# Optimization experiments

Hardware: AMD Instinct MI355X
Metric: run time of the kernel (lower is better)

The kernel has to match this reference:

```python
import jax, jax.numpy as jnp
import numpy as np

D_MODEL = 192
D_STATE = 16
D_CONV = 4
EXPAND = 2
HEADDIM = 16
D_INNER = EXPAND * D_MODEL          # 384
NHEADS = D_INNER // HEADDIM         # 24
NGROUPS = 1
CHUNK = 256
BATCH = 2
SEQLEN = 8192
D_IN_PROJ = 2 * D_INNER + NGROUPS * D_STATE + NHEADS   # 808
D_IN_PROJ_B = NGROUPS * D_STATE                         # 16
CONV_DIM = D_INNER + NGROUPS * D_STATE                  # 400
EPS = 1e-5


def silu(x):
    return x * jax.nn.sigmoid(x)


def causal_dwconv(x, w, b):
    # x: (B, L, C), w: (C, 1, K) depthwise, b: (C,). Causal: left-pad K-1.
    C = x.shape[-1]
    xt = jnp.transpose(x, (0, 2, 1))  # (B, C, L)
    y = jax.lax.conv_general_dilated(
        xt, w, window_strides=(1,), padding=[(D_CONV - 1, 0)],
        dimension_numbers=('NCH', 'OIH', 'NCH'), feature_group_count=C)
    return jnp.transpose(y + b[None, :, None], (0, 2, 1))


def segsum(x):
    # x: (..., T) -> (..., T, T) lower-triangular segment sums (exclusive of j, inclusive of i)
    T = x.shape[-1]
    cs = jnp.cumsum(x, axis=-1)
    seg = cs[..., :, None] - cs[..., None, :]
    mask = jnp.tril(jnp.ones((T, T), dtype=bool))
    return jnp.where(mask, seg, -jnp.inf)


def ssd(x, dt, A, Bm, Cm):
    # Mamba2 chunked selective scan (mamba_chunk_scan_combined semantics).
    # x:(b,l,h,p) dt:(b,l,h) A:(h,) Bm,Cm:(b,l,g,n)
    b, l, h, p = x.shape
    g = Bm.shape[2]
    Bm = jnp.repeat(Bm, h // g, axis=2)  # (b,l,h,n)
    Cm = jnp.repeat(Cm, h // g, axis=2)
    nchunks = l // CHUNK
    tochunk = lambda t: t.reshape(b, nchunks, CHUNK, *t.shape[2:])
    xc, dtc, Bc, Cc = map(tochunk, (x, dt, Bm, Cm))
    a = jnp.transpose(dtc * A, (0, 3, 1, 2))        # (b,h,c,cl)
    a_cum = jnp.cumsum(a, axis=-1)                   # (b,h,c,cl)
    Lmat = jnp.exp(segsum(a))                        # (b,h,c,cl,cl)
    xdt = xc * dtc[..., None]                        # (b,c,cl,h,p)
    # intra-chunk (diagonal) output
    Y_diag = jnp.einsum('bclhn,bcshn,bhcls,bcshp->bclhp', Cc, Bc, Lmat, xdt)
    # per-chunk end states
    decay_states = jnp.exp(a_cum[..., -1:] - a_cum)  # (b,h,c,cl)
    states = jnp.einsum('bclhn,bhcl,bclhp->bchpn', Bc, decay_states, xdt)
    # inter-chunk recurrence (associative, via chunk-level segsum)
    init = jnp.zeros_like(states[:, :1])
    states = jnp.concatenate([init, states], axis=1)              # (b,c+1,h,p,n)
    a_chunk = jnp.pad(a_cum[..., -1], ((0, 0), (0, 0), (1, 0)))   # (b,h,c+1)
    decay_chunk = jnp.exp(segsum(a_chunk))                        # (b,h,c+1,c+1)
    states = jnp.einsum('bhzc,bchpn->bzhpn', decay_chunk, states)[:, :-1]  # (b,c,h,p,n)
    # state -> output within each chunk
    Y_off = jnp.einsum('bclhn,bchpn,bhcl->bclhp', Cc, states, jnp.exp(a_cum))
    return (Y_diag + Y_off).reshape(b, l, h, p)


def setup_inputs() -> dict:
    key = jax.random.key(0)
    ks = jax.random.split(key, 12)
    rng = np.random.default_rng(0)
    u = jax.random.normal(ks[0], (BATCH, SEQLEN, D_MODEL), dtype=jnp.float32)
    support = jax.random.normal(ks[1], (BATCH, SEQLEN, D_MODEL), dtype=jnp.float32)
    W_in = jax.random.normal(ks[2], (D_IN_PROJ, D_MODEL), dtype=jnp.float32) * 0.02
    W_in_b = jax.random.normal(ks[3], (D_IN_PROJ_B, D_MODEL), dtype=jnp.float32) * 0.02
    conv_w = jax.random.normal(ks[4], (CONV_DIM, 1, D_CONV), dtype=jnp.float32) * 0.2
    conv_b = jnp.zeros((CONV_DIM,), dtype=jnp.float32)
    conv_w_b = jax.random.normal(ks[5], (D_IN_PROJ_B, 1, D_CONV), dtype=jnp.float32) * 0.2
    conv_b_b = jnp.zeros((D_IN_PROJ_B,), dtype=jnp.float32)
    # dt_bias init per the module (inverse-softplus of dt in [1e-3, 1e-1])
    dt = np.exp(rng.uniform(size=(NHEADS,)) * (np.log(0.1) - np.log(0.001)) + np.log(0.001))
    dt = np.clip(dt, 1e-4, None)
    dt_bias = jnp.asarray(dt + np.log(-np.expm1(-dt)), dtype=jnp.float32)
    A_log = jnp.asarray(np.log(rng.uniform(1.0, 16.0, size=(NHEADS,))), dtype=jnp.float32)
    D = jnp.ones((NHEADS,), dtype=jnp.float32)
    norm_w = jnp.ones((D_INNER,), dtype=jnp.float32)
    W_out = jax.random.normal(ks[6], (D_MODEL, D_INNER), dtype=jnp.float32) * 0.02
    return {'u': u, 'support': support, 'W_in': W_in, 'W_in_b': W_in_b,
            'conv_w': conv_w, 'conv_b': conv_b, 'conv_w_b': conv_w_b, 'conv_b_b': conv_b_b,
            'dt_bias': dt_bias, 'A_log': A_log, 'D': D, 'norm_w': norm_w, 'W_out': W_out}


def reference(u, support, W_in, W_in_b, conv_w, conv_b, conv_w_b, conv_b_b,
              dt_bias, A_log, D, norm_w, W_out):
    bsz, l, _ = u.shape
    zxbdt = u @ W_in.T                                  # (b,l,808)
    c = support @ W_in_b.T                              # (b,l,16)
    z = zxbdt[..., :D_INNER]
    xB = zxbdt[..., D_INNER:D_INNER + CONV_DIM]
    dt = jax.nn.softplus(zxbdt[..., -NHEADS:] + dt_bias)  # (b,l,h)
    A = -jnp.exp(A_log)
    xB = silu(causal_dwconv(xB, conv_w, conv_b))
    Cv = silu(causal_dwconv(c, conv_w_b, conv_b_b))
    x = xB[..., :D_INNER]
    Bv = xB[..., D_INNER:]
    xh = x.reshape(bsz, l, NHEADS, HEADDIM)
    Bg = Bv.reshape(bsz, l, NGROUPS, D_STATE)
    Cg = Cv.reshape(bsz, l, NGROUPS, D_STATE)
    y = ssd(xh, dt, A, Bg, Cg) + D[None, None, :, None] * xh
    y = y.reshape(bsz, l, D_INNER)
    # RMSNormGated, norm_before_gate=False: normalize(y * silu(z)) * weight
    yg = y * silu(z)
    yn = yg * jax.lax.rsqrt(jnp.mean(yg * yg, axis=-1, keepdims=True) + EPS) * norm_w
    return yn @ W_out.T
```

## Files before the change

kernel.cpp:

```cpp
#include <hip/hip_runtime.h>
#include <cmath>

#define ROWS      16384
#define SEQLEN    8192
#define BATCH     2
#define NHEADS    24
#define HEADDIM   16
#define D_STATE   16
#define D_INNER   384
#define D_MODEL   192
#define D_IN_PROJ 808
#define CONV_DIM  400
#define NCHUNKS   32
#define CHUNK     256
#define EPS       1e-5f
#define LOG2E     1.44269504088896f

typedef short bf16x8 __attribute__((ext_vector_type(8)));
typedef short bf16x4 __attribute__((ext_vector_type(4)));
typedef float f32x4  __attribute__((ext_vector_type(4)));
typedef unsigned short us4v __attribute__((ext_vector_type(4)));
typedef unsigned short us8v __attribute__((ext_vector_type(8)));
typedef unsigned int  u32x4 __attribute__((ext_vector_type(4)));

#if __has_builtin(__builtin_amdgcn_mfma_f32_16x16x16bf16_1k)
#define MFMA16(a, b, c) __builtin_amdgcn_mfma_f32_16x16x16bf16_1k((a), (b), (c), 0, 0, 0)
#define HAVE_MFMA16 1
#elif __has_builtin(__builtin_amdgcn_mfma_f32_16x16x16_bf16)
#define MFMA16(a, b, c) __builtin_amdgcn_mfma_f32_16x16x16_bf16((a), (b), (c), 0, 0, 0)
#define HAVE_MFMA16 1
#else
#define HAVE_MFMA16 0
#endif

__device__ __forceinline__ float silu_f(float x) { return x / (1.0f + expf(-x)); }
__device__ __forceinline__ float softplus_f(float x) { return (x > 20.0f) ? x : log1pf(expf(x)); }
__device__ __forceinline__ unsigned short f2bf(float x) {
  unsigned u = __builtin_bit_cast(unsigned, x);
  u += 0x7fff + ((u >> 16) & 1);
  return (unsigned short)(u >> 16);
}
__device__ __forceinline__ float bf2f(unsigned short s) {
  unsigned u = (unsigned)s << 16;
  return __builtin_bit_cast(float, u);
}
__device__ __forceinline__ unsigned pk_bf(float a, float b) {
  unsigned ua = __builtin_bit_cast(unsigned, a) + 0x7fffu;
  unsigned ub = __builtin_bit_cast(unsigned, b) + 0x7fffu;
  return __builtin_amdgcn_perm(ub, ua, 0x07060302u);
}

__global__ __launch_bounds__(256)
void cvt3_kernel(const float* __restrict__ a, unsigned short* __restrict__ ao, long na,
                 const float* __restrict__ b, unsigned short* __restrict__ bo, long nb,
                 const float* __restrict__ c, unsigned short* __restrict__ co, long nc) {
  const long t0 = na >> 2, t1 = t0 + (nb >> 2), t2 = t1 + (nc >> 2);
  const long stride = (long)gridDim.x * blockDim.x;
  for (long i = (long)blockIdx.x * blockDim.x + threadIdx.x; i < t2; i += stride) {
    const float4* s; us4v* d; long j;
    if (i < t0)      { s = (const float4*)a; d = (us4v*)ao; j = i; }
    else if (i < t1) { s = (const float4*)b; d = (us4v*)bo; j = i - t0; }
    else             { s = (const float4*)c; d = (us4v*)co; j = i - t1; }
    float4 v = s[j];
    us4v o = { f2bf(v.x), f2bf(v.y), f2bf(v.z), f2bf(v.w) };
    d[j] = o;
  }
}

template<bool OUT_BF16, bool ROUTE>
__device__ __forceinline__
void gemm_body(unsigned short* __restrict__ As, unsigned short* __restrict__ Ws,
               const float* __restrict__ A, const unsigned short* __restrict__ W,
               void* __restrict__ Cp, int M, int N, int K, int bx, int by,
               unsigned short* __restrict__ zbuf, unsigned short* __restrict__ xT,
               unsigned short* __restrict__ Braw, unsigned short* __restrict__ draw) {
  constexpr int BM = 128, BN = 128, BK = 32, LDK = 40;
  const int tid  = threadIdx.x;
  const int wid  = tid >> 6, lane = tid & 63;
  const int wr   = wid >> 1, wc = wid & 1;
  const int fr   = lane & 15, fq = lane >> 4;
  const long m0  = (long)by * BM;
  const int  n0  = bx * BN;

  f32x4 acc[4][4] = {};

  auto stage = [&](int k0, int buf) {
#pragma unroll
    for (int p = 0; p < 2; ++p) {
      int flat = p * 2048 + tid * 8;
      int r = flat >> 5, c = flat & 31;
      const float4* src = (const float4*)(A + (m0 + r) * (long)K + k0 + c);
      float4 v0 = src[0], v1 = src[1];
      us8v o = { f2bf(v0.x), f2bf(v0.y), f2bf(v0.z), f2bf(v0.w),
                 f2bf(v1.x), f2bf(v1.y), f2bf(v1.z), f2bf(v1.w) };
      *(us8v*)&As[buf * BM * LDK + r * LDK + c] = o;
    }
#pragma unroll
    for (int p = 0; p < 2; ++p) {
      int flat = p * 2048 + tid * 8;
      int r = flat >> 5, c = flat & 31;
      int gn = n0 + r;
      us8v v = { 0, 0, 0, 0, 0, 0, 0, 0 };
      if (gn < N) v = *(const us8v*)(W + (long)gn * K + k0 + c);
      *(us8v*)&Ws[buf * BN * LDK + r * LDK + c] = v;
    }
  };

  const int nk = K / BK;
  stage(0, 0);
  __syncthreads();
  for (int kt = 0; kt < nk; ++kt) {
    const int cur = kt & 1;
    if (kt + 1 < nk) stage((kt + 1) * BK, cur ^ 1);
    bf16x8 af[4], bfr[4];
#pragma unroll
    for (int m = 0; m < 4; ++m)
      af[m] = *(const bf16x8*)&As[cur * BM * LDK + (wr * 64 + m * 16 + fr) * LDK + fq * 8];
#pragma unroll
    for (int n = 0; n < 4; ++n)
      bfr[n] = *(const bf16x8*)&Ws[cur * BN * LDK + (wc * 64 + n * 16 + fr) * LDK + fq * 8];
#pragma unroll
    for (int m = 0; m < 4; ++m)
#pragma unroll
      for (int n = 0; n < 4; ++n)
        acc[m][n] = __builtin_amdgcn_mfma_f32_16x16x32_bf16(bfr[n], af[m], acc[m][n], 0, 0, 0);
    __syncthreads();
  }

#pragma unroll
  for (int m = 0; m < 4; ++m) {
    const long gm = m0 + wr * 64 + m * 16 + fr;
#pragma unroll
    for (int n = 0; n < 4; ++n) {
      const int gn = n0 + wc * 64 + n * 16 + fq * 4;
      if (gn < N) {
        if (ROUTE) {
          us4v o = { f2bf(acc[m][n][0]), f2bf(acc[m][n][1]),
                     f2bf(acc[m][n][2]), f2bf(acc[m][n][3]) };
          const int bb = (int)(gm >> 13);
          const long t = gm & 8191;
          if (gn < 384) {
            *(us4v*)(zbuf + gm * 384 + gn) = o;
          } else if (gn < 768) {
            const int c = gn - 384, hh = c >> 4, ii = c & 15;
            *(us4v*)(xT + (((size_t)(bb * NHEADS + hh) * SEQLEN + t) << 4) + ii) = o;
          } else if (gn < 784) {
            *(us4v*)(Braw + gm * 16 + (gn - 768)) = o;
          } else {
            *(us4v*)(draw + gm * 24 + (gn - 784)) = o;
          }
        } else if (OUT_BF16) {
          us4v o = { f2bf(acc[m][n][0]), f2bf(acc[m][n][1]),
                     f2bf(acc[m][n][2]), f2bf(acc[m][n][3]) };
          *(us4v*)((unsigned short*)Cp + gm * N + gn) = o;
        } else {
          float4 o = make_float4(acc[m][n][0], acc[m][n][1], acc[m][n][2], acc[m][n][3]);
          *(float4*)((float*)Cp + gm * N + gn) = o;
        }
      }
    }
  }
}

__global__ __launch_bounds__(256, 3)
void gemm_in_merged(const float* __restrict__ u, const unsigned short* __restrict__ Wi,
                    const float* __restrict__ support, const unsigned short* __restrict__ Wib,
                    unsigned short* __restrict__ craw,
                    unsigned short* __restrict__ zbuf, unsigned short* __restrict__ xT,
                    unsigned short* __restrict__ Braw, unsigned short* __restrict__ draw) {
  __shared__ unsigned short As[2 * 128 * 40];
  __shared__ unsigned short Ws[2 * 128 * 40];
  if (blockIdx.x < 7)
    gemm_body<true, true>(As, Ws, u, Wi, nullptr, ROWS, D_IN_PROJ, D_MODEL,
                          blockIdx.x, blockIdx.y, zbuf, xT, Braw, draw);
  else
    gemm_body<true, false>(As, Ws, support, Wib, craw, ROWS, D_STATE, D_MODEL,
                           0, blockIdx.y, nullptr, nullptr, nullptr, nullptr);
}

#define CBC_NB  (ROWS * 4 / 256)
#define CDT_NB  (ROWS * 3 / 256)

__global__ __launch_bounds__(256)
void conv_bcdt(const unsigned short* __restrict__ Braw, const unsigned short* __restrict__ craw,
               const unsigned short* __restrict__ draw,
               const float* __restrict__ conv_w, const float* __restrict__ conv_b,
               const float* __restrict__ conv_w_b, const float* __restrict__ conv_b_b,
               const float* __restrict__ dt_bias,
               unsigned short* __restrict__ Bo, unsigned short* __restrict__ Co,
               float* __restrict__ dtoT) {
  const int blk = blockIdx.x;
  const us8v z8 = { 0, 0, 0, 0, 0, 0, 0, 0 };

  if (blk < CBC_NB) {
    const int idx = blk * 256 + threadIdx.x;
    const int row = idx / 4, q = idx % 4;
    const int b = row / SEQLEN, t = row % SEQLEN;

    const unsigned short* src = (q < 2) ? Braw : craw;
    const float* cw = (q < 2) ? conv_w + 384 * 4 : conv_w_b;
    const float* cb = (q < 2) ? conv_b + 384 : conv_b_b;
    const int c0 = (q & 1) * 8;
    const unsigned short* base = src + (size_t)row * D_STATE + c0;
    us8v x0 = (t >= 3) ? *(const us8v*)(base - 3 * D_STATE) : z8;
    us8v x1 = (t >= 2) ? *(const us8v*)(base - 2 * D_STATE) : z8;
    us8v x2 = (t >= 1) ? *(const us8v*)(base - 1 * D_STATE) : z8;
    us8v x3 = *(const us8v*)base;
    us8v o;
#pragma unroll
    for (int ch = 0; ch < 8; ++ch) {
      const float4 wv = *(const float4*)(cw + (c0 + ch) * 4);
      float acc = cb[c0 + ch] + wv.x * bf2f(x0[ch]) + wv.y * bf2f(x1[ch])
                + wv.z * bf2f(x2[ch]) + wv.w * bf2f(x3[ch]);
      o[ch] = f2bf(silu_f(acc));
    }
    if (q < 2) *(us8v*)(Bo + (size_t)row * D_STATE + c0) = o;
    else       *(us8v*)(Co + (size_t)row * D_STATE + c0) = o;
  } else {
    const int idx = (blk - CBC_NB) * 256 + threadIdx.x;
    const int row = idx / 3, q = idx % 3;
    const int b = row / SEQLEN, t = row % SEQLEN;
    const int h0 = q * 8;
    us8v dv = *(const us8v*)(draw + (size_t)row * 24 + h0);
#pragma unroll
    for (int j = 0; j < 8; ++j) {
      float v = bf2f(dv[j]) + dt_bias[h0 + j];
      dtoT[(size_t)(b * NHEADS + h0 + j) * SEQLEN + t] = softplus_f(v);
    }
  }
}

__global__ __launch_bounds__(512, 4)
void ssd_mfma_kernel(const unsigned short* __restrict__ xT, const unsigned short* __restrict__ Bo,
                     const unsigned short* __restrict__ Co, const float* __restrict__ dtoT,
                     const float* __restrict__ A_log, const float* __restrict__ conv_w,
                     const float* __restrict__ conv_b, const float* __restrict__ Dvec,
                     unsigned short* __restrict__ YdT, float* __restrict__ acum_g,
                     float* __restrict__ csum_g, float* __restrict__ stloc) {
  const int bid  = blockIdx.x;
  const int wrk  = (bid & 7) * 192 + (bid >> 3);
  const int b    = wrk / 768;
  const int rem  = wrk % 768;
  const int cidx = rem / NHEADS;
  const int h    = rem % NHEADS;
  const int tid  = threadIdx.x;
  const int wid  = tid >> 6, lane = tid & 63;
  const int fr   = lane & 15, g = lane >> 4;

  __shared__ unsigned short Bs[256 * 24 + 32];
  __shared__ unsigned short xsT[16 * 264];
  __shared__ unsigned short BwT[16 * 264];
  __shared__ unsigned short xraw[259 * 16 + 8];
  __shared__ float sc2[CHUNK];
  __shared__ float scE[16];
  __shared__ float wsum[4];

  const float Ah = -expf(A_log[h]);
  const us8v z8 = { 0, 0, 0, 0, 0, 0, 0, 0 };

  float v = 0.f;
  if (tid < CHUNK) {
    v = dtoT[(size_t)(b * NHEADS + h) * SEQLEN + (size_t)cidx * CHUNK + tid] * Ah;
#pragma unroll
    for (int off = 1; off < 64; off <<= 1) {
      float u = __shfl_up(v, off, 64);
      if (lane >= off) v += u;
    }
    if (lane == 63) wsum[wid] = v;
  }

  const int r  = tid >> 1;
  const int hf = tid & 1;
  const size_t rowbase = (size_t)b * SEQLEN + (size_t)cidx * CHUNK;
  const size_t rhrow = (size_t)(b * NHEADS + h) * SEQLEN + (size_t)cidx * CHUNK + r;
  const float rdtv = dtoT[rhrow];
  us8v bh = ((const us8v*)(Bo + (rowbase + r) * D_STATE))[hf];
  if (hf == 0) *(us8v*)&Bs[r * 24 + 16] = z8;
  if (tid < 32) Bs[256 * 24 + tid] = 0;
  {
    const int tg = cidx * CHUNK + r - 3;
    us8v xv = z8;
    if (tg >= 0)
      xv = *(const us8v*)(xT + (((size_t)(b * NHEADS + h) * SEQLEN + tg) << 4) + 8 * hf);
    *(us8v*)&xraw[r * 16 + 8 * hf] = xv;
    if (tid < 6) {
      const int rr2 = 256 + (tid >> 1);
      const int hf2 = tid & 1;
      const int tg2 = cidx * CHUNK + rr2 - 3;
      us8v xv2 = *(const us8v*)(xT + (((size_t)(b * NHEADS + h) * SEQLEN + tg2) << 4) + 8 * hf2);
      *(us8v*)&xraw[rr2 * 16 + 8 * hf2] = xv2;
    }
  }
  __syncthreads();

  us8v xsil, xdt8;
  {
    us8v tA = *(const us8v*)&xraw[(r + 0) * 16 + 8 * hf];
    us8v tB = *(const us8v*)&xraw[(r + 1) * 16 + 8 * hf];
    us8v tC = *(const us8v*)&xraw[(r + 2) * 16 + 8 * hf];
    us8v tD = *(const us8v*)&xraw[(r + 3) * 16 + 8 * hf];
    const int cbase = h * HEADDIM + 8 * hf;
#pragma unroll
    for (int ch = 0; ch < 8; ++ch) {
      const float4 wv = *(const float4*)(conv_w + (cbase + ch) * 4);
      float acc = conv_b[cbase + ch] + wv.x * bf2f(tA[ch]) + wv.y * bf2f(tB[ch])
                + wv.z * bf2f(tC[ch]) + wv.w * bf2f(tD[ch]);
      float sv = silu_f(acc);
      xsil[ch] = f2bf(sv);
      xdt8[ch] = f2bf(sv * rdtv);
    }
  }
  const float ctot  = wsum[0] + wsum[1] + wsum[2] + wsum[3];
  const float ctot2 = ctot * LOG2E;
  if (tid < CHUNK) {
    float pre = 0.f;
#pragma unroll
    for (int w = 0; w < 4; ++w) if (w < wid) pre += wsum[w];
    v += pre;
    sc2[tid] = v * LOG2E;
    acum_g[(size_t)(b * NHEADS + h) * SEQLEN + (size_t)cidx * CHUNK + tid] = v;
    if (tid == CHUNK - 1) csum_g[(b * NHEADS + h) * NCHUNKS + cidx] = v;
  }
  __syncthreads();

  *(us8v*)&xraw[(r + 3) * 16 + 8 * hf] = xsil;
#pragma unroll
  for (int q = 0; q < 8; ++q)
    xsT[(q + 8 * hf) * 264 + r] = xdt8[q];
  {
    const float wdv = exp2f(ctot2 - sc2[r]);
    const float ed  = exp2f(sc2[r | 15] - sc2[r]);
    us8v bscaled;
#pragma unroll
    for (int q = 0; q < 8; ++q) {
      BwT[(q + 8 * hf) * 264 + r] = f2bf(bf2f(bh[q]) * wdv);
      bscaled[q] = f2bf(bf2f(bh[q]) * ed);
    }
    *(us8v*)&Bs[r * 24 + 8 * hf] = bscaled;
  }
  if (tid < 16) scE[tid] = sc2[tid * 16 + 15];
  __syncthreads();

  if (wid == 0) {
    f32x4 accS = {};
#pragma unroll
    for (int k2 = 0; k2 < 8; ++k2) {
      bf16x8 af = *(const bf16x8*)&BwT[fr * 264 + 32 * k2 + 8 * g];
      bf16x8 bb = *(const bf16x8*)&xsT[fr * 264 + 32 * k2 + 8 * g];
      accS = __builtin_amdgcn_mfma_f32_16x16x32_bf16(af, bb, accS, 0, 0, 0);
    }
    *(f32x4*)&stloc[((size_t)(b * NCHUNKS + cidx) * NHEADS + h) * 256 + fr * 16 + 4 * g] = accS;
  }

  const f32x4 zf = { 0.f, 0.f, 0.f, 0.f };
  const unsigned short* Cbase = Co + rowbase * D_STATE;
  const float Dh = Dvec[h];
  const int strips[2] = { wid, 15 - wid };

  bf16x8 brawq[2];
#pragma unroll
  for (int q = 0; q < 2; ++q) {
    us8v bv = z8;
    if (g < 2)
      bv = *(const us8v*)(Bo + (rowbase + strips[q] * 16 + fr) * D_STATE + 8 * g);
    brawq[q] = __builtin_bit_cast(bf16x8, bv);
  }

#if HAVE_MFMA16
#pragma unroll
  for (int q = 0; q < 2; ++q) {
    const int lt = strips[q];
    f32x4 acc = zf;
    bf16x8 cf = { 0, 0, 0, 0, 0, 0, 0, 0 };
    if (g < 2) cf = *(const bf16x8*)(Cbase + (size_t)(lt * 16 + fr) * D_STATE + 8 * g);
    const float acl2 = sc2[lt * 16 + fr];
    const int   lg   = lt * 16 + fr;
    for (int st = 0; st <= lt; ++st) {
      uint2 pp;
      if (st < lt) {
        bf16x8 bfg = *(const bf16x8*)&Bs[(st * 16 + fr) * 24 + 8 * g];
        f32x4 G = __builtin_amdgcn_mfma_f32_16x16x32_bf16(bfg, cf, zf, 0, 0, 0);
        const float wl = exp2f(acl2 - scE[st]);
        pp.x = pk_bf(G[0] * wl, G[1] * wl);
        pp.y = pk_bf(G[2] * wl, G[3] * wl);
      } else {
        f32x4 G = __builtin_amdgcn_mfma_f32_16x16x32_bf16(brawq[q], cf, zf, 0, 0, 0);
        f32x4 se2 = *(const f32x4*)&sc2[st * 16 + 4 * g];
        const int sbase = st * 16 + 4 * g;
        float w0 = (sbase + 0 <= lg) ? exp2f(acl2 - se2[0]) : 0.f;
        float w1 = (sbase + 1 <= lg) ? exp2f(acl2 - se2[1]) : 0.f;
        float w2 = (sbase + 2 <= lg) ? exp2f(acl2 - se2[2]) : 0.f;
        float w3 = (sbase + 3 <= lg) ? exp2f(acl2 - se2[3]) : 0.f;
        pp.x = pk_bf(G[0] * w0, G[1] * w1);
        pp.y = pk_bf(G[2] * w2, G[3] * w3);
      }
      const bf16x4 p4 = __builtin_bit_cast(bf16x4, pp);
      const bf16x4 x4 = *(const bf16x4*)&xsT[fr * 264 + st * 16 + 4 * g];
      acc = MFMA16(x4, p4, acc);
    }
    us4v xs4 = *(const us4v*)&xraw[(lt * 16 + fr + 3) * 16 + 4 * g];
    us4v o = { f2bf(acc[0] + Dh * bf2f(xs4[0])),
               f2bf(acc[1] + Dh * bf2f(xs4[1])),
               f2bf(acc[2] + Dh * bf2f(xs4[2])),
               f2bf(acc[3] + Dh * bf2f(xs4[3])) };
    *(us4v*)(YdT + (rhrow - r + (size_t)lt * 16 + fr) * HEADDIM + 4 * g) = o;
  }
#else
  const int Ls0 = fr + ((g & 1) << 5);
  const int Ls1 = Ls0 + 16;
  const bool hiq = (g >= 2);
#pragma unroll
  for (int q = 0; q < 2; ++q) {
    const int lt = strips[q];
    f32x4 acc = zf;
    bf16x8 cf = { 0, 0, 0, 0, 0, 0, 0, 0 };
    if (g < 2) cf = *(const bf16x8*)(Cbase + (size_t)(lt * 16 + fr) * D_STATE + 8 * g);
    const float acl2 = sc2[lt * 16 + fr];
    const int   lg   = lt * 16 + fr;
    const int npair = (lt + 2) >> 1;
    for (int sp = 0; sp < npair; ++sp) {
      uint2 pk[2];
#pragma unroll
      for (int ti = 0; ti < 2; ++ti) {
        const int st = 2 * sp + ti;
        if (st < lt) {
          bf16x8 bfg = *(const bf16x8*)&Bs[(st * 16 + fr) * 24 + 8 * g];
          f32x4 G = __builtin_amdgcn_mfma_f32_16x16x32_bf16(bfg, cf, zf, 0, 0, 0);
          const float wl = exp2f(acl2 - scE[st]);
          pk[ti].x = pk_bf(G[0] * wl, G[1] * wl);
          pk[ti].y = pk_bf(G[2] * wl, G[3] * wl);
        } else if (st == lt) {
          f32x4 G = __builtin_amdgcn_mfma_f32_16x16x32_bf16(brawq[q], cf, zf, 0, 0, 0);
          f32x4 se2 = *(const f32x4*)&sc2[st * 16 + 4 * g];
          const int sbase = st * 16 + 4 * g;
          float w0 = (sbase + 0 <= lg) ? exp2f(acl2 - se2[0]) : 0.f;
          float w1 = (sbase + 1 <= lg) ? exp2f(acl2 - se2[1]) : 0.f;
          float w2 = (sbase + 2 <= lg) ? exp2f(acl2 - se2[2]) : 0.f;
          float w3 = (sbase + 3 <= lg) ? exp2f(acl2 - se2[3]) : 0.f;
          pk[ti].x = pk_bf(G[0] * w0, G[1] * w1);
          pk[ti].y = pk_bf(G[2] * w2, G[3] * w3);
        } else {
          pk[ti].x = 0u; pk[ti].y = 0u;
        }
      }
      const int a00 = __shfl((int)pk[0].x, Ls0, 64);
      const int a10 = __shfl((int)pk[0].y, Ls0, 64);
      const int a01 = __shfl((int)pk[0].x, Ls1, 64);
      const int a11 = __shfl((int)pk[0].y, Ls1, 64);
      const int b00 = __shfl((int)pk[1].x, Ls0, 64);
      const int b10 = __shfl((int)pk[1].y, Ls0, 64);
      const int b01 = __shfl((int)pk[1].x, Ls1, 64);
      const int b11 = __shfl((int)pk[1].y, Ls1, 64);
      u32x4 pw;
      pw[0] = (unsigned)(hiq ? b00 : a00);
      pw[1] = (unsigned)(hiq ? b10 : a10);
      pw[2] = (unsigned)(hiq ? b01 : a01);
      pw[3] = (unsigned)(hiq ? b11 : a11);
      const bf16x8 pf = __builtin_bit_cast(bf16x8, pw);
      const bf16x8 xf = *(const bf16x8*)&xsT[fr * 264 + sp * 32 + 8 * g];
      acc = __builtin_amdgcn_mfma_f32_16x16x32_bf16(xf, pf, acc, 0, 0, 0);
    }
    us4v xs4 = *(const us4v*)&xraw[(lt * 16 + fr + 3) * 16 + 4 * g];
    us4v o = { f2bf(acc[0] + Dh * bf2f(xs4[0])),
               f2bf(acc[1] + Dh * bf2f(xs4[1])),
               f2bf(acc[2] + Dh * bf2f(xs4[2])),
               f2bf(acc[3] + Dh * bf2f(xs4[3])) };
    *(us4v*)(YdT + (rhrow - r + (size_t)lt * 16 + fr) * HEADDIM + 4 * g) = o;
  }
#endif
}

__global__ __launch_bounds__(256)
void chunk_scan_kernel(const float* __restrict__ stloc, const float* __restrict__ csum_g,
                       float* __restrict__ stpre) {
  const int b  = blockIdx.x / NHEADS;
  const int h  = blockIdx.x % NHEADS;
  const int pn = threadIdx.x;
  float S = 0.0f;
  for (int c = 0; c < NCHUNKS; ++c) {
    const size_t idx = ((size_t)(b * NCHUNKS + c) * NHEADS + h) * 256 + pn;
    stpre[idx] = S;
    S = __expf(csum_g[(b * NHEADS + h) * NCHUNKS + c]) * S + stloc[idx];
  }
}

#define TT 16
#define LDY 392
__global__ __launch_bounds__(768)
void yoff_norm_gemm(const unsigned short* __restrict__ YdT,
                    const unsigned short* __restrict__ Co, const float* __restrict__ acum_g,
                    const float* __restrict__ stpre,
                    const unsigned short* __restrict__ zbuf, const float* __restrict__ norm_w,
                    const unsigned short* __restrict__ Wo,
                    float* __restrict__ out) {
  const int bid  = blockIdx.x;
  const int wz   = (bid & 7) * 128 + (bid >> 3);
  const int r0   = wz * TT;
  const int b    = r0 / SEQLEN;
  const int t0   = r0 % SEQLEN;
  const int cidx = t0 / CHUNK;
  const int tid  = threadIdx.x;
  const int d    = tid % 384;
  const int half = tid / 384;
  const int h    = d >> 4, p = d & 15;
  const int wv   = tid >> 6;

  __shared__ unsigned short Yt[NHEADS * TT * 16];
  __shared__ unsigned short zL[TT * 384];
  __shared__ unsigned short ynL[TT * LDY];
  __shared__ float At[NHEADS * TT];
  __shared__ float Ct[TT * 16];
  __shared__ float red[TT][8];

  {
    us8v* Yt8 = (us8v*)Yt;
    int hh = tid >> 5, q = tid & 31;
    const size_t src = ((size_t)(b * NHEADS + hh) * SEQLEN + t0) * HEADDIM + q * 8;
    Yt8[tid] = *(const us8v*)(YdT + src);
    const int zr = tid / 48, zc = (tid % 48) * 8;
    *(us8v*)&zL[zr * 384 + zc] = *(const us8v*)(zbuf + (size_t)(r0 + zr) * 384 + zc);
    if (tid < NHEADS * TT)
      At[tid] = __expf(acum_g[(size_t)(b * NHEADS + (tid >> 4)) * SEQLEN + t0 + (tid & 15)]);
    if (tid < TT * 16) Ct[tid] = bf2f(Co[(size_t)r0 * D_STATE + tid]);
    if (tid < TT * 2) red[tid >> 1][6 + (tid & 1)] = 0.f;
  }

  f32x4 S4[4];
  {
    const float* Sp = stpre + ((size_t)(b * NCHUNKS + cidx) * NHEADS + h) * 256 + p * 16;
#pragma unroll
    for (int q = 0; q < 4; ++q) S4[q] = *(const f32x4*)(Sp + 4 * q);
  }
  const float nw = norm_w[d];
  __syncthreads();

  const int tb = half * 8;
#pragma unroll
  for (int ti = 0; ti < 8; ++ti) {
    const int tt = tb + ti;
    const f32x4* C4 = (const f32x4*)&Ct[tt * 16];
    f32x4 d4 = C4[0] * S4[0];
    d4 = d4 + C4[1] * S4[1];
    d4 = d4 + C4[2] * S4[2];
    d4 = d4 + C4[3] * S4[3];
    const float dot = (d4[0] + d4[1]) + (d4[2] + d4[3]);
    const float eA = At[h * TT + tt];
    float y = bf2f(Yt[h * 256 + tt * 16 + p]) + eA * dot;
    const float z = bf2f(zL[tt * 384 + d]);
    const float yg = y * silu_f(z);
    ynL[tt * LDY + d] = f2bf(yg * nw);
    float s = yg * yg;
#pragma unroll
    for (int off = 32; off > 0; off >>= 1) s += __shfl_down(s, off);
    if ((tid & 63) == 0) red[tt][wv - half * 6] = s;
  }
  __syncthreads();

  const int lane = tid & 63;
  const int fr = lane & 15, fq = lane >> 4;
  const int n0 = wv * 16;
  const f32x4 r4 = *(const f32x4*)&red[fr][0];
  const float tot = ((r4[0] + r4[1]) + (r4[2] + r4[3])) + (red[fr][4] + red[fr][5]);
  const float scale = rsqrtf(tot * (1.0f / D_INNER) + EPS);
  f32x4 accg = {};
  __builtin_amdgcn_s_setprio(1);
#pragma unroll
  for (int kt = 0; kt < 12; ++kt) {
    const bf16x8 af = *(const bf16x8*)&ynL[fr * LDY + kt * 32 + 8 * fq];
    const int col = n0 + fr;
    const bf16x8 bfr = *(const bf16x8*)(Wo + (size_t)col * D_INNER + kt * 32 + 8 * fq);
    accg = __builtin_amdgcn_mfma_f32_16x16x32_bf16(bfr, af, accg, 0, 0, 0);
  }
  __builtin_amdgcn_s_setprio(0);
  float4 o = make_float4(accg[0] * scale, accg[1] * scale,
                         accg[2] * scale, accg[3] * scale);
  *(float4*)(out + (size_t)(r0 + fr) * D_MODEL + n0 + fq * 4) = o;
}

extern "C" void kernel_launch(void* const* d_in, const int* in_sizes, int n_in,
                              void* d_out, int out_size, void* d_ws, size_t ws_size,
                              hipStream_t stream) {
  const float* u        = (const float*)d_in[0];
  const float* support  = (const float*)d_in[1];
  const float* W_in     = (const float*)d_in[2];
  const float* W_in_b   = (const float*)d_in[3];
  const float* conv_w   = (const float*)d_in[4];
  const float* conv_b   = (const float*)d_in[5];
  const float* conv_w_b = (const float*)d_in[6];
  const float* conv_b_b = (const float*)d_in[7];
  const float* dt_bias  = (const float*)d_in[8];
  const float* A_log    = (const float*)d_in[9];
  const float* Dvec     = (const float*)d_in[10];
  const float* norm_w   = (const float*)d_in[11];
  const float* W_out    = (const float*)d_in[12];
  float* out = (float*)d_out;
  char* wsb  = (char*)d_ws;

  unsigned short* Wi_b  = (unsigned short*)(wsb);
  unsigned short* Wo_b  = Wi_b + (size_t)D_IN_PROJ * D_MODEL;
  unsigned short* Wib_b = Wo_b + (size_t)D_MODEL * D_INNER;
  unsigned short* zbuf  = Wib_b + (size_t)D_STATE * D_MODEL;
  unsigned short* xT    = zbuf + (size_t)ROWS * D_INNER;
  unsigned short* Braw  = xT + (size_t)ROWS * D_INNER;
  unsigned short* draw  = Braw + (size_t)ROWS * D_STATE;
  unsigned short* craw  = draw + (size_t)ROWS * NHEADS;
  unsigned short* Bo    = craw + (size_t)ROWS * D_STATE;
  unsigned short* Co    = Bo + (size_t)ROWS * D_STATE;
  unsigned short* YdT   = Co + (size_t)ROWS * D_STATE;
  float* dtoT  = (float*)(YdT + (size_t)ROWS * D_INNER);
  float* acum  = dtoT  + (size_t)ROWS * NHEADS;
  float* csum  = acum  + (size_t)BATCH * NHEADS * SEQLEN;
  float* stloc = csum  + (size_t)BATCH * NHEADS * NCHUNKS;
  float* stpre = stloc + (size_t)BATCH * NCHUNKS * NHEADS * 256;

  cvt3_kernel<<<224, 256, 0, stream>>>(W_in, Wi_b, (long)D_IN_PROJ * D_MODEL,
                                       W_out, Wo_b, (long)D_MODEL * D_INNER,
                                       W_in_b, Wib_b, (long)D_STATE * D_MODEL);
  gemm_in_merged<<<dim3(8, ROWS / 128), 256, 0, stream>>>(
      u, Wi_b, support, Wib_b, craw, zbuf, xT, Braw, draw);
  conv_bcdt<<<CBC_NB + CDT_NB, 256, 0, stream>>>(
      Braw, craw, draw, conv_w, conv_b, conv_w_b, conv_b_b, dt_bias, Bo, Co, dtoT);
  ssd_mfma_kernel<<<NHEADS * NCHUNKS * BATCH, 512, 0, stream>>>(
      xT, Bo, Co, dtoT, A_log, conv_w, conv_b, Dvec, YdT, acum, csum, stloc);
  chunk_scan_kernel<<<BATCH * NHEADS, 256, 0, stream>>>(stloc, csum, stpre);
  yoff_norm_gemm<<<ROWS / TT, 768, 0, stream>>>(YdT, Co, acum, stpre, zbuf, norm_w,
                                                Wo_b, out);
}
```

Before: 113.3 us.

## Fold norm weight into W_out and compute RMS sum via MFMA Gram diagonal

```diff
diff --git a/kernel.cpp b/kernel.cpp
--- a/kernel.cpp
+++ b/kernel.cpp
@@ -53,17 +53,29 @@
 __global__ __launch_bounds__(256)
 void cvt3_kernel(const float* __restrict__ a, unsigned short* __restrict__ ao, long na,
                  const float* __restrict__ b, unsigned short* __restrict__ bo, long nb,
-                 const float* __restrict__ c, unsigned short* __restrict__ co, long nc) {
+                 const float* __restrict__ c, unsigned short* __restrict__ co, long nc,
+                 const float* __restrict__ nwp) {
   const long t0 = na >> 2, t1 = t0 + (nb >> 2), t2 = t1 + (nc >> 2);
   const long stride = (long)gridDim.x * blockDim.x;
   for (long i = (long)blockIdx.x * blockDim.x + threadIdx.x; i < t2; i += stride) {
-    const float4* s; us4v* d; long j;
-    if (i < t0)      { s = (const float4*)a; d = (us4v*)ao; j = i; }
-    else if (i < t1) { s = (const float4*)b; d = (us4v*)bo; j = i - t0; }
-    else             { s = (const float4*)c; d = (us4v*)co; j = i - t1; }
-    float4 v = s[j];
-    us4v o = { f2bf(v.x), f2bf(v.y), f2bf(v.z), f2bf(v.w) };
-    d[j] = o;
+    if (i < t0) {
+      float4 v = ((const float4*)a)[i];
+      us4v o = { f2bf(v.x), f2bf(v.y), f2bf(v.z), f2bf(v.w) };
+      ((us4v*)ao)[i] = o;
+    } else if (i < t1) {
+      const long j = i - t0;
+      float4 v = ((const float4*)b)[j];
+      const int d0 = (int)((j * 4) % D_INNER);
+      const float4 nw4 = *(const float4*)(nwp + d0);
+      us4v o = { f2bf(v.x * nw4.x), f2bf(v.y * nw4.y),
+                 f2bf(v.z * nw4.z), f2bf(v.w * nw4.w) };
+      ((us4v*)bo)[j] = o;
+    } else {
+      const long j = i - t1;
+      float4 v = ((const float4*)c)[j];
+      us4v o = { f2bf(v.x), f2bf(v.y), f2bf(v.z), f2bf(v.w) };
+      ((us4v*)co)[j] = o;
+    }
   }
 }
 
@@ -490,7 +502,7 @@
 void yoff_norm_gemm(const unsigned short* __restrict__ YdT,
                     const unsigned short* __restrict__ Co, const float* __restrict__ acum_g,
                     const float* __restrict__ stpre,
-                    const unsigned short* __restrict__ zbuf, const float* __restrict__ norm_w,
+                    const unsigned short* __restrict__ zbuf,
                     const unsigned short* __restrict__ Wo,
                     float* __restrict__ out) {
   const int bid  = blockIdx.x;
@@ -510,7 +522,6 @@
   __shared__ unsigned short ynL[TT * LDY];
   __shared__ float At[NHEADS * TT];
   __shared__ float Ct[TT * 16];
-  __shared__ float red[TT][8];
 
   {
     us8v* Yt8 = (us8v*)Yt;
@@ -522,7 +533,6 @@
     if (tid < NHEADS * TT)
       At[tid] = __expf(acum_g[(size_t)(b * NHEADS + (tid >> 4)) * SEQLEN + t0 + (tid & 15)]);
     if (tid < TT * 16) Ct[tid] = bf2f(Co[(size_t)r0 * D_STATE + tid]);
-    if (tid < TT * 2) red[tid >> 1][6 + (tid & 1)] = 0.f;
   }
 
   f32x4 S4[4];
@@ -531,7 +541,6 @@
 #pragma unroll
     for (int q = 0; q < 4; ++q) S4[q] = *(const f32x4*)(Sp + 4 * q);
   }
-  const float nw = norm_w[d];
   __syncthreads();
 
   const int tb = half * 8;
@@ -547,31 +556,29 @@
     const float eA = At[h * TT + tt];
     float y = bf2f(Yt[h * 256 + tt * 16 + p]) + eA * dot;
     const float z = bf2f(zL[tt * 384 + d]);
-    const float yg = y * silu_f(z);
-    ynL[tt * LDY + d] = f2bf(yg * nw);
-    float s = yg * yg;
-#pragma unroll
-    for (int off = 32; off > 0; off >>= 1) s += __shfl_down(s, off);
-    if ((tid & 63) == 0) red[tt][wv - half * 6] = s;
+    ynL[tt * LDY + d] = f2bf(y * silu_f(z));
   }
   __syncthreads();
 
   const int lane = tid & 63;
   const int fr = lane & 15, fq = lane >> 4;
   const int n0 = wv * 16;
-  const f32x4 r4 = *(const f32x4*)&red[fr][0];
-  const float tot = ((r4[0] + r4[1]) + (r4[2] + r4[3])) + (red[fr][4] + red[fr][5]);
-  const float scale = rsqrtf(tot * (1.0f / D_INNER) + EPS);
   f32x4 accg = {};
+  f32x4 gacc = {};
   __builtin_amdgcn_s_setprio(1);
 #pragma unroll
   for (int kt = 0; kt < 12; ++kt) {
     const bf16x8 af = *(const bf16x8*)&ynL[fr * LDY + kt * 32 + 8 * fq];
-    const int col = n0 + fr;
-    const bf16x8 bfr = *(const bf16x8*)(Wo + (size_t)col * D_INNER + kt * 32 + 8 * fq);
+    const bf16x8 bfr = *(const bf16x8*)(Wo + (size_t)(n0 + fr) * D_INNER + kt * 32 + 8 * fq);
     accg = __builtin_amdgcn_mfma_f32_16x16x32_bf16(bfr, af, accg, 0, 0, 0);
+    gacc = __builtin_amdgcn_mfma_f32_16x16x32_bf16(af, af, gacc, 0, 0, 0);
   }
   __builtin_amdgcn_s_setprio(0);
+  const int j0 = fr & 3;
+  float vsel = (j0 == 0) ? gacc[0] : (j0 == 1) ? gacc[1]
+             : (j0 == 2) ? gacc[2] : gacc[3];
+  const float tot = __shfl(vsel, (fr >> 2) * 16 + fr, 64);
+  const float scale = rsqrtf(tot * (1.0f / D_INNER) + EPS);
   float4 o = make_float4(accg[0] * scale, accg[1] * scale,
                          accg[2] * scale, accg[3] * scale);
   *(float4*)(out + (size_t)(r0 + fr) * D_MODEL + n0 + fq * 4) = o;
@@ -615,7 +622,8 @@
 
   cvt3_kernel<<<224, 256, 0, stream>>>(W_in, Wi_b, (long)D_IN_PROJ * D_MODEL,
                                        W_out, Wo_b, (long)D_MODEL * D_INNER,
-                                       W_in_b, Wib_b, (long)D_STATE * D_MODEL);
+                                       W_in_b, Wib_b, (long)D_STATE * D_MODEL,
+                                       norm_w);
   gemm_in_merged<<<dim3(8, ROWS / 128), 256, 0, stream>>>(
       u, Wi_b, support, Wib_b, craw, zbuf, xT, Braw, draw);
   conv_bcdt<<<CBC_NB + CDT_NB, 256, 0, stream>>>(
@@ -623,6 +631,6 @@
   ssd_mfma_kernel<<<NHEADS * NCHUNKS * BATCH, 512, 0, stream>>>(
       xT, Bo, Co, dtoT, A_log, conv_w, conv_b, Dvec, YdT, acum, csum, stloc);
   chunk_scan_kernel<<<BATCH * NHEADS, 256, 0, stream>>>(stloc, csum, stpre);
-  yoff_norm_gemm<<<ROWS / TT, 768, 0, stream>>>(YdT, Co, acum, stpre, zbuf, norm_w,
+  yoff_norm_gemm<<<ROWS / TT, 768, 0, stream>>>(YdT, Co, acum, stpre, zbuf,
                                                 Wo_b, out);
 }
```

New measurement: 106.6 us. 1.06x faster.
